# Kernel tuning notes

Hardware: AMD Instinct MI355X
Metric: run time of the kernel (lower is better)

Reference implementation:

```python
import jax, jax.numpy as jnp
import numpy as np

NUM_EXPERTS = 8
TOP_K = 2
NUM_TOKENS = 16384  # bs*slen = 4*4096
DIM = 4096


def setup_inputs() -> dict:
    key = jax.random.key(0)
    k1, k2 = jax.random.split(key)
    x = jax.random.normal(k1, (NUM_TOKENS, DIM), dtype=jnp.float32)
    # gate = nn.Linear(dim, num_experts, bias=False): weight shape [num_experts, dim]
    W = jax.random.normal(k2, (NUM_EXPERTS, DIM), dtype=jnp.float32) * 0.02
    return {"x": x, "W": W}


def reference(x, W):
    # gate linear: scores [T, E]
    logits = jnp.einsum("td,ed->te", x, W)
    # softmax=False path: sigmoid in fp32, cast back to input dtype
    scores = jax.nn.sigmoid(logits.astype(jnp.float32)).astype(x.dtype)
    # top-k experts per token
    top_scores, selected_experts = jax.lax.top_k(scores, TOP_K)  # [T, K]
    # norm_topk_prob = False -> no renormalization
    flat_experts = selected_experts.reshape(-1)  # [T*K]
    # histc(bins=E, min=0, max=E) on int indices in [0, E) == bincount
    num_tokens_per_expert = jnp.bincount(flat_experts, length=NUM_EXPERTS)
    # stable argsort by expert id -> dispatch permutation
    order = jnp.argsort(flat_experts, stable=True)  # [T*K]
    top_scores_sorted = top_scores.reshape(-1)[order]
    token_indices = order // TOP_K
    return top_scores_sorted, token_indices, num_tokens_per_expert
```

## Files before the change

### kernel.cpp

```cpp
#include <hip/hip_runtime.h>
#include <hip/hip_bf16.h>

#define NUM_TOKENS 16384
#define DIM 4096
#define NE 8
#define NSLOTS (NUM_TOKENS * 2)
#define NB1 256
#define NB2 128

typedef unsigned long long u64;

__device__ __forceinline__ void onehot_add(u64& h0, u64& h1, int e) {
    if (e < 4) h0 += 1ull << (16 * e);
    else       h1 += 1ull << (16 * (e - 4));
}
__device__ __forceinline__ unsigned field_of(u64 h0, u64 h1, int e) {
    return (unsigned)(((e < 4) ? (h0 >> (16 * e)) : (h1 >> (16 * (e - 4)))) & 0xFFFFull);
}

__global__ __launch_bounds__(1024) void router_fused(
    const float* __restrict__ x, const float* __restrict__ W,
    float* __restrict__ scores_ws,
    u64* __restrict__ pr_ws,
    u64* __restrict__ bh_ws)
{
    __shared__ float4 Wlds[NE * (DIM / 4)];
    __shared__ int eLds[128];

    const int tid = threadIdx.x;
    const int lane = tid & 63;
    const int wave = tid >> 6;
    const int tok0 = blockIdx.x * 64 + wave * 4;

    const float4* x4 = reinterpret_cast<const float4*>(x);
    const float4* xr0 = x4 + (size_t)(tok0 + 0) * (DIM / 4);
    const float4* xr1 = x4 + (size_t)(tok0 + 1) * (DIM / 4);
    const float4* xr2 = x4 + (size_t)(tok0 + 2) * (DIM / 4);
    const float4* xr3 = x4 + (size_t)(tok0 + 3) * (DIM / 4);

    float4 p0 = xr0[lane];
    float4 p1 = xr1[lane];
    float4 p2 = xr2[lane];
    float4 p3 = xr3[lane];

    const float4* W4 = reinterpret_cast<const float4*>(W);
#pragma unroll
    for (int k = 0; k < 8; ++k)
        Wlds[tid + k * 1024] = W4[tid + k * 1024];
    __syncthreads();

    float a[32];
#pragma unroll
    for (int v = 0; v < 32; ++v) a[v] = 0.f;

#define GEMV_STEP(XA, XB, XC, XD, F4I)                                          \
    do {                                                                        \
        _Pragma("unroll")                                                       \
        for (int e = 0; e < 8; ++e) {                                           \
            float4 w = Wlds[e * 1024 + (F4I)];                                  \
            a[0*8+e] = fmaf((XA).w, w.w, fmaf((XA).z, w.z, fmaf((XA).y, w.y, fmaf((XA).x, w.x, a[0*8+e])))); \
            a[1*8+e] = fmaf((XB).w, w.w, fmaf((XB).z, w.z, fmaf((XB).y, w.y, fmaf((XB).x, w.x, a[1*8+e])))); \
            a[2*8+e] = fmaf((XC).w, w.w, fmaf((XC).z, w.z, fmaf((XC).y, w.y, fmaf((XC).x, w.x, a[2*8+e])))); \
            a[3*8+e] = fmaf((XD).w, w.w, fmaf((XD).z, w.z, fmaf((XD).y, w.y, fmaf((XD).x, w.x, a[3*8+e])))); \
        }                                                                       \
    } while (0)

    GEMV_STEP(p0, p1, p2, p3, lane);
#pragma unroll 3
    for (int it = 1; it < 16; ++it) {
        const int f4i = it * 64 + lane;
        float4 xa = xr0[f4i];
        float4 xb = xr1[f4i];
        float4 xc = xr2[f4i];
        float4 xd = xr3[f4i];
        GEMV_STEP(xa, xb, xc, xd, f4i);
    }

#define MERGE(DST, A, B, BIT, DIST)                       \
    do {                                                  \
        const bool sel = (lane >> (BIT)) & 1;             \
        float _lo = sel ? (B) : (A);                      \
        float _hi = sel ? (A) : (B);                      \
        DST = _lo + __shfl_xor(_hi, (DIST), 64);          \
    } while (0)

    float m1[16], m2[8], m3[4], m4[2], m5;
#pragma unroll
    for (int i = 0; i < 16; ++i) MERGE(m1[i], a[2*i], a[2*i+1], 0, 1);
#pragma unroll
    for (int i = 0; i < 8; ++i)  MERGE(m2[i], m1[2*i], m1[2*i+1], 1, 2);
#pragma unroll
    for (int i = 0; i < 4; ++i)  MERGE(m3[i], m2[2*i], m2[2*i+1], 2, 4);
#pragma unroll
    for (int i = 0; i < 2; ++i)  MERGE(m4[i], m3[2*i], m3[2*i+1], 3, 8);
    MERGE(m5, m4[0], m4[1], 4, 16);
    m5 += __shfl_xor(m5, 32, 64);

    const float s = 1.0f / (1.0f + expf(-m5));

    float v1 = s; int e1 = lane & 7;
#pragma unroll
    for (int d = 1; d < 8; d <<= 1) {
        float ov = __shfl_xor(v1, d, 64);
        int   oe = __shfl_xor(e1, d, 64);
        const bool take = (ov > v1) || (ov == v1 && oe < e1);
        v1 = take ? ov : v1;
        e1 = take ? oe : e1;
    }
    float v2 = ((lane & 7) == e1) ? -1e30f : s; int e2 = lane & 7;
#pragma unroll
    for (int d = 1; d < 8; d <<= 1) {
        float ov = __shfl_xor(v2, d, 64);
        int   oe = __shfl_xor(e2, d, 64);
        const bool take = (ov > v2) || (ov == v2 && oe < e2);
        v2 = take ? ov : v2;
        e2 = take ? oe : e2;
    }

    if ((lane & 7) == 0 && lane < 32) {
        const int t = lane >> 3;
        const int tok = tok0 + t;
        reinterpret_cast<float2*>(scores_ws)[tok] = make_float2(v1, v2);
        reinterpret_cast<int2*>(eLds)[wave * 4 + t] = make_int2(e1, e2);
    }
    __syncthreads();

    if (wave == 0) {
        const int2 ee = reinterpret_cast<const int2*>(eLds)[lane];
        u64 h0 = 0ull, h1 = 0ull;
        onehot_add(h0, h1, ee.x);
        onehot_add(h0, h1, ee.y);
        const u64 own0 = h0, own1 = h1;
#pragma unroll
        for (int d = 1; d < 64; d <<= 1) {
            u64 n0 = __shfl_up(h0, d, 64);
            u64 n1 = __shfl_up(h1, d, 64);
            if (lane >= d) { h0 += n0; h1 += n1; }
        }
        u64 ex0 = h0 - own0, ex1 = h1 - own1;
        const unsigned rankA = field_of(ex0, ex1, ee.x);
        onehot_add(ex0, ex1, ee.x);
        const unsigned rankB = field_of(ex0, ex1, ee.y);
        const u64 packed = (u64)(rankA | ((unsigned)ee.x << 16)) |
                           ((u64)(rankB | ((unsigned)ee.y << 16)) << 32);
        pr_ws[blockIdx.x * 64 + lane] = packed;

        const u64 t0 = __shfl(h0, 63, 64);
        const u64 t1 = __shfl(h1, 63, 64);
        if (lane == 0) {
            bh_ws[2 * blockIdx.x + 0] = t0;
            bh_ws[2 * blockIdx.x + 1] = t1;
        }
    }
}

__global__ __launch_bounds__(256) void router_scatter(
    const float* __restrict__ scores_ws,
    const u64* __restrict__ pr_ws,
    const u64* __restrict__ bh_ws,
    float* __restrict__ out)
{
    __shared__ u64 offsLds[4];
    __shared__ float totLds[NE];

    const int tid = threadIdx.x;
    const int lane = tid & 63;
    const int wave = tid >> 6;
    const int b = blockIdx.x;

    if (wave == 0) {
        const ulonglong2* bh2 = reinterpret_cast<const ulonglong2*>(bh_ws);
        const ulonglong2 hA = bh2[4 * lane + 0];
        const ulonglong2 hB = bh2[4 * lane + 1];
        const ulonglong2 hC = bh2[4 * lane + 2];
        const ulonglong2 hD = bh2[4 * lane + 3];

        const u64 ex1_0 = hA.x,         ex1_1 = hA.y;
        const u64 ex2_0 = ex1_0 + hB.x, ex2_1 = ex1_1 + hB.y;
        const u64 ex3_0 = ex2_0 + hC.x, ex3_1 = ex2_1 + hC.y;
        const u64 inc0  = ex3_0 + hD.x, inc1  = ex3_1 + hD.y;

        u64 s0 = inc0, s1 = inc1;
#pragma unroll
        for (int d = 1; d < 64; d <<= 1) {
            u64 n0 = __shfl_up(s0, d, 64);
            u64 n1 = __shfl_up(s1, d, 64);
            if (lane >= d) { s0 += n0; s1 += n1; }
        }
        const u64 base0 = s0 - inc0, base1 = s1 - inc1;
        const u64 g0 = __shfl(s0, 63, 64);
        const u64 g1 = __shfl(s1, 63, 64);

        unsigned t0e = (unsigned)((g0 >>  0) & 0xFFFF), t1e = (unsigned)((g0 >> 16) & 0xFFFF);
        unsigned t2e = (unsigned)((g0 >> 32) & 0xFFFF), t3e = (unsigned)((g0 >> 48) & 0xFFFF);
        unsigned t4e = (unsigned)((g1 >>  0) & 0xFFFF), t5e = (unsigned)((g1 >> 16) & 0xFFFF);
        unsigned t6e = (unsigned)((g1 >> 32) & 0xFFFF);
        unsigned b0 = 0, b1 = b0 + t0e, b2 = b1 + t1e, b3 = b2 + t2e;
        unsigned b4 = b3 + t3e, b5 = b4 + t4e, b6 = b5 + t5e, b7 = b6 + t6e;
        const u64 pb0 = (u64)b0 | ((u64)b1 << 16) | ((u64)b2 << 32) | ((u64)b3 << 48);
        const u64 pb1 = (u64)b4 | ((u64)b5 << 16) | ((u64)b6 << 32) | ((u64)b7 << 48);

        if (lane == (b >> 1)) {
            u64 x0_0, x0_1, x1_0, x1_1;
            if (b & 1) { x0_0 = ex2_0; x0_1 = ex2_1; x1_0 = ex3_0; x1_1 = ex3_1; }
            else       { x0_0 = 0ull;  x0_1 = 0ull;  x1_0 = ex1_0; x1_1 = ex1_1; }
            offsLds[0] = base0 + x0_0 + pb0;
            offsLds[1] = base1 + x0_1 + pb1;
            offsLds[2] = base0 + x1_0 + pb0;
            offsLds[3] = base1 + x1_1 + pb1;
        }
        if (lane < NE) {
            const unsigned tv = (unsigned)((((lane < 4) ? (g0 >> (16 * lane))
                                                        : (g1 >> (16 * (lane - 4)))) & 0xFFFFull));
            totLds[lane] = (float)tv;
        }
    }
    __syncthreads();

    if (b == 0 && tid < NE) out[2 * NSLOTS + tid] = totLds[tid];

    const int s = b * 256 + tid;
    const unsigned pr = reinterpret_cast<const unsigned*>(pr_ws)[s];
    const unsigned rank = pr & 0xFFFFu;
    const int e = (int)(pr >> 16);
    const int half = tid >> 7;
    const u64 o0 = offsLds[2 * half + 0];
    const u64 o1 = offsLds[2 * half + 1];
    const unsigned p = field_of(o0, o1, e) + rank;

    out[p] = scores_ws[s];
    out[NSLOTS + p] = (float)(s >> 1);
}

extern "C" void kernel_launch(void* const* d_in, const int* in_sizes, int n_in,
                              void* d_out, int out_size, void* d_ws, size_t ws_size,
                              hipStream_t stream) {
    const float* x = (const float*)d_in[0];
    const float* W = (const float*)d_in[1];
    float* out = (float*)d_out;

    char* ws = (char*)d_ws;
    float* scores_ws = (float*)(ws);
    u64*   pr_ws     = (u64*)(ws + (1 << 17));
    u64*   bh_ws     = (u64*)(ws + (1 << 18));

    router_fused<<<NB1, 1024, 0, stream>>>(x, W, scores_ws, pr_ws, bh_ws);
    router_scatter<<<NB2, 256, 0, stream>>>(scores_ws, pr_ws, bh_ws, out);
}
```

Baseline: 55.27 us.

## Fuse router and scatter kernels via cooperative grid sync

Merges the two kernels into one cooperative launch. Scores and per-token ranks stay in LDS and registers, a grid-wide barrier follows the per-block histogram write, and each block then computes its own offsets and scatters its tokens directly. This removes a kernel launch and the workspace round trip for scores and packed ranks. In exchange it adds the cost of a grid sync and requires all 256 blocks of 1024 threads to be co-resident. The scatter step now runs on a single wave per block.

```diff
diff --git a/kernel.cpp b/kernel.cpp
--- a/kernel.cpp
+++ b/kernel.cpp
@@ -1,12 +1,11 @@
 #include <hip/hip_runtime.h>
-#include <hip/hip_bf16.h>
+#include <hip/hip_cooperative_groups.h>
 
 #define NUM_TOKENS 16384
 #define DIM 4096
 #define NE 8
 #define NSLOTS (NUM_TOKENS * 2)
 #define NB1 256
-#define NB2 128
 
 typedef unsigned long long u64;
 
@@ -18,19 +17,20 @@
     return (unsigned)(((e < 4) ? (h0 >> (16 * e)) : (h1 >> (16 * (e - 4)))) & 0xFFFFull);
 }
 
-__global__ __launch_bounds__(1024) void router_fused(
+__global__ __launch_bounds__(1024) void router_all(
     const float* __restrict__ x, const float* __restrict__ W,
-    float* __restrict__ scores_ws,
-    u64* __restrict__ pr_ws,
-    u64* __restrict__ bh_ws)
+    u64* __restrict__ bh_ws,
+    float* __restrict__ out)
 {
     __shared__ float4 Wlds[NE * (DIM / 4)];
-    __shared__ int eLds[128];
+    __shared__ int   eLds[128];
+    __shared__ float sLds[128];
 
     const int tid = threadIdx.x;
     const int lane = tid & 63;
     const int wave = tid >> 6;
-    const int tok0 = blockIdx.x * 64 + wave * 4;
+    const int b = blockIdx.x;
+    const int tok0 = b * 64 + wave * 4;
 
     const float4* x4 = reinterpret_cast<const float4*>(x);
     const float4* xr0 = x4 + (size_t)(tok0 + 0) * (DIM / 4);
@@ -118,15 +118,16 @@
     }
 
     if ((lane & 7) == 0 && lane < 32) {
-        const int t = lane >> 3;
-        const int tok = tok0 + t;
-        reinterpret_cast<float2*>(scores_ws)[tok] = make_float2(v1, v2);
-        reinterpret_cast<int2*>(eLds)[wave * 4 + t] = make_int2(e1, e2);
+        const int tl = wave * 4 + (lane >> 3);
+        reinterpret_cast<float2*>(sLds)[tl] = make_float2(v1, v2);
+        reinterpret_cast<int2*>(eLds)[tl]   = make_int2(e1, e2);
     }
     __syncthreads();
 
+    int2 ee = make_int2(0, 0);
+    unsigned rankA = 0, rankB = 0;
     if (wave == 0) {
-        const int2 ee = reinterpret_cast<const int2*>(eLds)[lane];
+        ee = reinterpret_cast<const int2*>(eLds)[lane];
         u64 h0 = 0ull, h1 = 0ull;
         onehot_add(h0, h1, ee.x);
         onehot_add(h0, h1, ee.y);
@@ -138,35 +139,20 @@
             if (lane >= d) { h0 += n0; h1 += n1; }
         }
         u64 ex0 = h0 - own0, ex1 = h1 - own1;
-        const unsigned rankA = field_of(ex0, ex1, ee.x);
+        rankA = field_of(ex0, ex1, ee.x);
         onehot_add(ex0, ex1, ee.x);
-        const unsigned rankB = field_of(ex0, ex1, ee.y);
-        const u64 packed = (u64)(rankA | ((unsigned)ee.x << 16)) |
-                           ((u64)(rankB | ((unsigned)ee.y << 16)) << 32);
-        pr_ws[blockIdx.x * 64 + lane] = packed;
+        rankB = field_of(ex0, ex1, ee.y);
 
         const u64 t0 = __shfl(h0, 63, 64);
         const u64 t1 = __shfl(h1, 63, 64);
         if (lane == 0) {
-            bh_ws[2 * blockIdx.x + 0] = t0;
-            bh_ws[2 * blockIdx.x + 1] = t1;
-        }
-    }
-}
-
-__global__ __launch_bounds__(256) void router_scatter(
-    const float* __restrict__ scores_ws,
-    const u64* __restrict__ pr_ws,
-    const u64* __restrict__ bh_ws,
-    float* __restrict__ out)
-{
-    __shared__ u64 offsLds[4];
-    __shared__ float totLds[NE];
-
-    const int tid = threadIdx.x;
-    const int lane = tid & 63;
-    const int wave = tid >> 6;
-    const int b = blockIdx.x;
+            bh_ws[2 * b + 0] = t0;
+            bh_ws[2 * b + 1] = t1;
+        }
+    }
+
+    __threadfence();
+    cooperative_groups::this_grid().sync();
 
     if (wave == 0) {
         const ulonglong2* bh2 = reinterpret_cast<const ulonglong2*>(bh_ws);
@@ -175,10 +161,10 @@
         const ulonglong2 hC = bh2[4 * lane + 2];
         const ulonglong2 hD = bh2[4 * lane + 3];
 
-        const u64 ex1_0 = hA.x,         ex1_1 = hA.y;
-        const u64 ex2_0 = ex1_0 + hB.x, ex2_1 = ex1_1 + hB.y;
-        const u64 ex3_0 = ex2_0 + hC.x, ex3_1 = ex2_1 + hC.y;
-        const u64 inc0  = ex3_0 + hD.x, inc1  = ex3_1 + hD.y;
+        const u64 x1_0 = hA.x,         x1_1 = hA.y;
+        const u64 x2_0 = x1_0 + hB.x,  x2_1 = x1_1 + hB.y;
+        const u64 x3_0 = x2_0 + hC.x,  x3_1 = x2_1 + hC.y;
+        const u64 inc0 = x3_0 + hD.x,  inc1 = x3_1 + hD.y;
 
         u64 s0 = inc0, s1 = inc1;
 #pragma unroll
@@ -200,36 +186,32 @@
         const u64 pb0 = (u64)b0 | ((u64)b1 << 16) | ((u64)b2 << 32) | ((u64)b3 << 48);
         const u64 pb1 = (u64)b4 | ((u64)b5 << 16) | ((u64)b6 << 32) | ((u64)b7 << 48);
 
-        if (lane == (b >> 1)) {
-            u64 x0_0, x0_1, x1_0, x1_1;
-            if (b & 1) { x0_0 = ex2_0; x0_1 = ex2_1; x1_0 = ex3_0; x1_1 = ex3_1; }
-            else       { x0_0 = 0ull;  x0_1 = 0ull;  x1_0 = ex1_0; x1_1 = ex1_1; }
-            offsLds[0] = base0 + x0_0 + pb0;
-            offsLds[1] = base1 + x0_1 + pb1;
-            offsLds[2] = base0 + x1_0 + pb0;
-            offsLds[3] = base1 + x1_1 + pb1;
-        }
-        if (lane < NE) {
-            const unsigned tv = (unsigned)((((lane < 4) ? (g0 >> (16 * lane))
-                                                        : (g1 >> (16 * (lane - 4)))) & 0xFFFFull));
-            totLds[lane] = (float)tv;
-        }
-    }
-    __syncthreads();
-
-    if (b == 0 && tid < NE) out[2 * NSLOTS + tid] = totLds[tid];
-
-    const int s = b * 256 + tid;
-    const unsigned pr = reinterpret_cast<const unsigned*>(pr_ws)[s];
-    const unsigned rank = pr & 0xFFFFu;
-    const int e = (int)(pr >> 16);
-    const int half = tid >> 7;
-    const u64 o0 = offsLds[2 * half + 0];
-    const u64 o1 = offsLds[2 * half + 1];
-    const unsigned p = field_of(o0, o1, e) + rank;
-
-    out[p] = scores_ws[s];
-    out[NSLOTS + p] = (float)(s >> 1);
+        const int owner = b >> 2, sub = b & 3;
+        u64 sel0, sel1;
+        switch (sub) {
+            case 0:  sel0 = base0 + pb0;        sel1 = base1 + pb1;        break;
+            case 1:  sel0 = base0 + x1_0 + pb0; sel1 = base1 + x1_1 + pb1; break;
+            case 2:  sel0 = base0 + x2_0 + pb0; sel1 = base1 + x2_1 + pb1; break;
+            default: sel0 = base0 + x3_0 + pb0; sel1 = base1 + x3_1 + pb1; break;
+        }
+        const u64 o0 = __shfl(sel0, owner, 64);
+        const u64 o1 = __shfl(sel1, owner, 64);
+
+        if (b == 0 && lane < NE) {
+            const unsigned tv = (unsigned)(((lane < 4) ? (g0 >> (16 * lane))
+                                                       : (g1 >> (16 * (lane - 4)))) & 0xFFFFull);
+            out[2 * NSLOTS + lane] = (float)tv;
+        }
+
+        const float2 sc = reinterpret_cast<const float2*>(sLds)[lane];
+        const float tokf = (float)(b * 64 + lane);
+        const unsigned pA = field_of(o0, o1, ee.x) + rankA;
+        const unsigned pB = field_of(o0, o1, ee.y) + rankB;
+        out[pA] = sc.x;
+        out[NSLOTS + pA] = tokf;
+        out[pB] = sc.y;
+        out[NSLOTS + pB] = tokf;
+    }
 }
 
 extern "C" void kernel_launch(void* const* d_in, const int* in_sizes, int n_in,
@@ -238,12 +220,9 @@
     const float* x = (const float*)d_in[0];
     const float* W = (const float*)d_in[1];
     float* out = (float*)d_out;
-
-    char* ws = (char*)d_ws;
-    float* scores_ws = (float*)(ws);
-    u64*   pr_ws     = (u64*)(ws + (1 << 17));
-    u64*   bh_ws     = (u64*)(ws + (1 << 18));
-
-    router_fused<<<NB1, 1024, 0, stream>>>(x, W, scores_ws, pr_ws, bh_ws);
-    router_scatter<<<NB2, 256, 0, stream>>>(scores_ws, pr_ws, bh_ws, out);
-}
+    u64* bh_ws = (u64*)d_ws;
+
+    void* args[] = { (void*)&x, (void*)&W, (void*)&bh_ws, (void*)&out };
+    hipLaunchCooperativeKernel(reinterpret_cast<void*>(router_all),
+                               dim3(NB1), dim3(1024), args, 0, stream);
+}
```

After: 145.3 us. 2.63x slower.
